# Kernel optimization log

Hardware: AMD Instinct MI355X
Metric: run time of the kernel (lower is better)

Reference implementation:

```python
import jax, jax.numpy as jnp
import numpy as np
import math

B, S, E, H = 2, 4096, 1024, 1024

def setup_inputs() -> dict:
    key = jax.random.key(0)
    ks = jax.random.split(key, 7)
    X = jax.random.normal(ks[0], (B, S, E), dtype=jnp.float32)
    attention_mask = jnp.ones((B, S, S), dtype=jnp.int32)
    sc = 1.0 / math.sqrt(E)
    Wq = jax.random.normal(ks[1], (H, E), dtype=jnp.float32) * sc
    Wk = jax.random.normal(ks[2], (H, E), dtype=jnp.float32) * sc
    Wv = jax.random.normal(ks[3], (H, E), dtype=jnp.float32) * sc
    bq = jnp.zeros((H,), dtype=jnp.float32)
    bk = jnp.zeros((H,), dtype=jnp.float32)
    bv = jnp.zeros((H,), dtype=jnp.float32)
    return {"X": X, "attention_mask": attention_mask,
            "Wq": Wq, "bq": bq, "Wk": Wk, "bk": bk, "Wv": Wv, "bv": bv}

def reference(X, attention_mask, Wq, bq, Wk, bk, Wv, bv):
    # Linear layers: y = x @ W^T + b (torch convention W is [out, in])
    Q = jnp.einsum('bse,he->bsh', X, Wq) + bq
    K = jnp.einsum('bse,he->bsh', X, Wk) + bk
    V = jnp.einsum('bse,he->bsh', X, Wv) + bv
    scale = 1.0 / math.sqrt(H)
    scores = jnp.einsum('bqh,bkh->bqk', Q, K) * scale  # [B,S,S]
    scores = jnp.where(attention_mask == 0, -jnp.inf, scores)
    # dropout (eval mode -> identity) would be applied here, BEFORE softmax
    weights = jax.nn.softmax(scores, axis=-1)
    out = jnp.einsum('bqk,bkh->bqh', weights, V)  # [B,S,H]
    return out
```

## Files before the change

kernel.cpp:

```cpp
#include <hip/hip_runtime.h>
#include <stdint.h>


typedef __bf16 bf16;
typedef __attribute__((ext_vector_type(4))) __bf16 bf16x4;
typedef __attribute__((ext_vector_type(8))) __bf16 bf16x8;
typedef __attribute__((ext_vector_type(4))) float f32x4;

__device__ __forceinline__ void g2l16(const void* g, void* l) {
  __builtin_amdgcn_global_load_lds(
      (const __attribute__((address_space(1))) uint32_t*)g,
      (__attribute__((address_space(3))) uint32_t*)l, 16, 0, 0);
}

__global__ __launch_bounds__(256) void cvt_f32_bf16(
    const float* __restrict__ src, bf16* __restrict__ dst, int n) {
  const int i = (blockIdx.x * 256 + threadIdx.x) * 8;
  if (i >= n) return;
  f32x4 a = *(const f32x4*)(src + i);
  f32x4 b = *(const f32x4*)(src + i + 4);
  bf16x8 o;
#pragma unroll
  for (int e = 0; e < 4; ++e) { o[e] = (bf16)a[e]; o[4 + e] = (bf16)b[e]; }
  *(bf16x8*)(dst + i) = o;
}

__global__ __launch_bounds__(256) void cvt_w3(
    const float* __restrict__ Wq, const float* __restrict__ Wk,
    const float* __restrict__ Wv, bf16* __restrict__ dst) {
  const int i = (blockIdx.x * 256 + threadIdx.x) * 8;
  const int seg = i >> 20;
  const int off = i & 1048575;
  const float* src = (seg == 0) ? Wq : (seg == 1) ? Wk : Wv;
  f32x4 a = *(const f32x4*)(src + off);
  f32x4 b = *(const f32x4*)(src + off + 4);
  bf16x8 o;
#pragma unroll
  for (int e = 0; e < 4; ++e) { o[e] = (bf16)a[e]; o[4 + e] = (bf16)b[e]; }
  *(bf16x8*)(dst + i) = o;
}


__global__ __launch_bounds__(256, 2) void gemm_qkv(
    const bf16* __restrict__ Xb, const bf16* __restrict__ Wb3,
    const float* __restrict__ bq, const float* __restrict__ bk,
    const float* __restrict__ bv, bf16* __restrict__ QK,
    bf16* __restrict__ Vt)
{
  constexpr int K = 1024, N = 1024;
  __shared__ __align__(16) bf16 ldsA[128 * 64];
  __shared__ __align__(16) bf16 ldsB[128 * 64];

  const int tid  = threadIdx.x;
  const int lane = tid & 63;
  const int wave = tid >> 6;
  const int which = blockIdx.y >> 3;
  const int n0 = (blockIdx.y & 7) * 128;
  const int m0 = blockIdx.x * 128;
  const bf16* Bt = Wb3 + (size_t)which * 1048576;
  const float* bias = (which == 0) ? bq : ((which == 1) ? bk : bv);

  const int l15  = lane & 15;
  const int quad = lane >> 4;
  const int wm = (wave >> 1) * 64;
  const int wn = (wave & 1) * 64;
  const int sw = l15 & 7;

  f32x4 acc[4][4];
#pragma unroll
  for (int i = 0; i < 4; ++i)
#pragma unroll
    for (int j = 0; j < 4; ++j) acc[i][j] = f32x4{0.f, 0.f, 0.f, 0.f};

  const int srow = tid >> 3;
  const int scol = ((tid & 7) ^ (srow & 7)) * 8;
  const size_t a_base = (size_t)(m0 + srow) * K + scol;
  const size_t b_base = (size_t)(n0 + srow) * K + scol;
  const int lds_off = tid * 8;

  for (int kt = 0; kt < K; kt += 64) {
    const bf16* ga = Xb + a_base + kt;
    const bf16* gb = Bt + b_base + kt;
#pragma unroll
    for (int it = 0; it < 4; ++it) {
      g2l16(ga + (size_t)(it * 32) * K, &ldsA[lds_off + it * 2048]);
      g2l16(gb + (size_t)(it * 32) * K, &ldsB[lds_off + it * 2048]);
    }
    __syncthreads();
#pragma unroll
    for (int ks = 0; ks < 2; ++ks) {
      const int ch = ks * 4 + quad;
      bf16x8 af[4], bfg[4];
#pragma unroll
      for (int i = 0; i < 4; ++i)
        af[i] = *(const bf16x8*)&ldsA[(wm + i * 16 + l15) * 64 + (ch ^ sw) * 8];
#pragma unroll
      for (int j = 0; j < 4; ++j)
        bfg[j] = *(const bf16x8*)&ldsB[(wn + j * 16 + l15) * 64 + (ch ^ sw) * 8];
#pragma unroll
      for (int i = 0; i < 4; ++i)
#pragma unroll
        for (int j = 0; j < 4; ++j)
          acc[i][j] = __builtin_amdgcn_mfma_f32_16x16x32_bf16(
              af[i], bfg[j], acc[i][j], 0, 0, 0);
    }
    __syncthreads();
  }

  if (which < 2) {
    bf16* C = QK + (size_t)which * (size_t)(8192 * 1024);
#pragma unroll
    for (int i = 0; i < 4; ++i) {
#pragma unroll
      for (int j = 0; j < 4; ++j) {
        const int r = m0 + wm + i * 16 + quad * 4;
        const int c = n0 + wn + j * 16 + l15;
        const float bvv = bias[c];
        f32x4 v = acc[i][j];
#pragma unroll
        for (int reg = 0; reg < 4; ++reg)
          C[(size_t)(r + reg) * N + c] = (bf16)(v[reg] + bvv);
      }
    }
  } else {
#pragma unroll
    for (int i = 0; i < 4; ++i) {
#pragma unroll
      for (int j = 0; j < 4; ++j) {
        const int r = m0 + wm + i * 16 + quad * 4;
        const int c = n0 + wn + j * 16 + l15;
        const int b = r >> 12, s = r & 4095;
        const float bvv = bias[c];
        f32x4 v = acc[i][j];
        bf16x4 o;
#pragma unroll
        for (int reg = 0; reg < 4; ++reg) o[reg] = (bf16)(v[reg] + bvv);
        *(bf16x4*)&Vt[((size_t)(b * 1024 + c)) * 4096 + s] = o;
      }
    }
  }
}

__global__ __launch_bounds__(256, 2) void gemm_scores(
    const bf16* __restrict__ A, const bf16* __restrict__ Bt,
    const int* __restrict__ mask, bf16* __restrict__ P,
    float* __restrict__ row_sum)
{
  constexpr int N = 4096, K = 1024;
  __shared__ __align__(16) bf16 ldsA[128 * 64];
  __shared__ __align__(16) bf16 ldsB[128 * 64];

  const int tid  = threadIdx.x;
  const int lane = tid & 63;
  const int wave = tid >> 6;
  const int m0 = blockIdx.x * 128;
  const int n0 = blockIdx.y * 128;
  const int batch = m0 >> 12;
  const bf16* Btb = Bt + (size_t)batch * (size_t)(4096 * 1024);

  const int l15  = lane & 15;
  const int quad = lane >> 4;
  const int wm = (wave >> 1) * 64;
  const int wn = (wave & 1) * 64;
  const int sw = l15 & 7;

  f32x4 acc[4][4];
#pragma unroll
  for (int i = 0; i < 4; ++i)
#pragma unroll
    for (int j = 0; j < 4; ++j) acc[i][j] = f32x4{0.f, 0.f, 0.f, 0.f};

  const int srow = tid >> 3;
  const int scol = ((tid & 7) ^ (srow & 7)) * 8;
  const size_t a_base = (size_t)(m0 + srow) * K + scol;
  const size_t b_base = (size_t)(n0 + srow) * K + scol;
  const int lds_off = tid * 8;

  for (int kt = 0; kt < K; kt += 64) {
    const bf16* ga = A + a_base + kt;
    const bf16* gb = Btb + b_base + kt;
#pragma unroll
    for (int it = 0; it < 4; ++it) {
      g2l16(ga + (size_t)(it * 32) * K, &ldsA[lds_off + it * 2048]);
      g2l16(gb + (size_t)(it * 32) * K, &ldsB[lds_off + it * 2048]);
    }
    __syncthreads();
#pragma unroll
    for (int ks = 0; ks < 2; ++ks) {
      const int ch = ks * 4 + quad;
      bf16x8 af[4], bfg[4];
#pragma unroll
      for (int i = 0; i < 4; ++i)
        af[i] = *(const bf16x8*)&ldsA[(wm + i * 16 + l15) * 64 + (ch ^ sw) * 8];
#pragma unroll
      for (int j = 0; j < 4; ++j)
        bfg[j] = *(const bf16x8*)&ldsB[(wn + j * 16 + l15) * 64 + (ch ^ sw) * 8];
#pragma unroll
      for (int i = 0; i < 4; ++i)
#pragma unroll
        for (int j = 0; j < 4; ++j)
          acc[i][j] = __builtin_amdgcn_mfma_f32_16x16x32_bf16(
              af[i], bfg[j], acc[i][j], 0, 0, 0);
    }
    __syncthreads();
  }

#pragma unroll
  for (int i = 0; i < 4; ++i) {
    const int r = m0 + wm + i * 16 + quad * 4;
    f32x4 rsum = f32x4{0.f, 0.f, 0.f, 0.f};
#pragma unroll
    for (int j = 0; j < 4; ++j) {
      const int c = n0 + wn + j * 16 + l15;
      f32x4 v = acc[i][j];
#pragma unroll
      for (int reg = 0; reg < 4; ++reg) {
        float e = __expf(v[reg] * 0.03125f);
        if (mask[(size_t)(r + reg) * N + c] == 0) e = 0.f;
        P[(size_t)(r + reg) * N + c] = (bf16)e;
        rsum[reg] += e;
      }
    }
#pragma unroll
    for (int off = 1; off < 16; off <<= 1) {
#pragma unroll
      for (int reg = 0; reg < 4; ++reg)
        rsum[reg] += __shfl_xor(rsum[reg], off);
    }
    if (l15 == 0) {
#pragma unroll
      for (int reg = 0; reg < 4; ++reg)
        atomicAdd(&row_sum[r + reg], rsum[reg]);
    }
  }
}

__global__ __launch_bounds__(256, 2) void gemm_pv(
    const bf16* __restrict__ A, const bf16* __restrict__ Bt,
    const float* __restrict__ row_sum, float* __restrict__ C)
{
  constexpr int N = 1024, K = 4096;
  __shared__ __align__(16) bf16 ldsA[128 * 64];
  __shared__ __align__(16) bf16 ldsB[128 * 64];

  const int tid  = threadIdx.x;
  const int lane = tid & 63;
  const int wave = tid >> 6;
  const int m0 = blockIdx.x * 128;
  const int n0 = blockIdx.y * 128;
  const int batch = m0 >> 12;
  const bf16* Btb = Bt + (size_t)batch * (size_t)(1024 * 4096);

  const int l15  = lane & 15;
  const int quad = lane >> 4;
  const int wm = (wave >> 1) * 64;
  const int wn = (wave & 1) * 64;
  const int sw = l15 & 7;

  f32x4 acc[4][4];
#pragma unroll
  for (int i = 0; i < 4; ++i)
#pragma unroll
    for (int j = 0; j < 4; ++j) acc[i][j] = f32x4{0.f, 0.f, 0.f, 0.f};

  const int srow = tid >> 3;
  const int scol = ((tid & 7) ^ (srow & 7)) * 8;
  const size_t a_base = (size_t)(m0 + srow) * K + scol;
  const size_t b_base = (size_t)(n0 + srow) * K + scol;
  const int lds_off = tid * 8;

  for (int kt = 0; kt < K; kt += 64) {
    const bf16* ga = A + a_base + kt;
    const bf16* gb = Btb + b_base + kt;
#pragma unroll
    for (int it = 0; it < 4; ++it) {
      g2l16(ga + (size_t)(it * 32) * K, &ldsA[lds_off + it * 2048]);
      g2l16(gb + (size_t)(it * 32) * K, &ldsB[lds_off + it * 2048]);
    }
    __syncthreads();
#pragma unroll
    for (int ks = 0; ks < 2; ++ks) {
      const int ch = ks * 4 + quad;
      bf16x8 af[4], bfg[4];
#pragma unroll
      for (int i = 0; i < 4; ++i)
        af[i] = *(const bf16x8*)&ldsA[(wm + i * 16 + l15) * 64 + (ch ^ sw) * 8];
#pragma unroll
      for (int j = 0; j < 4; ++j)
        bfg[j] = *(const bf16x8*)&ldsB[(wn + j * 16 + l15) * 64 + (ch ^ sw) * 8];
#pragma unroll
      for (int i = 0; i < 4; ++i)
#pragma unroll
        for (int j = 0; j < 4; ++j)
          acc[i][j] = __builtin_amdgcn_mfma_f32_16x16x32_bf16(
              af[i], bfg[j], acc[i][j], 0, 0, 0);
    }
    __syncthreads();
  }

#pragma unroll
  for (int i = 0; i < 4; ++i) {
    const int r = m0 + wm + i * 16 + quad * 4;
    f32x4 inv;
#pragma unroll
    for (int reg = 0; reg < 4; ++reg) inv[reg] = 1.0f / row_sum[r + reg];
#pragma unroll
    for (int j = 0; j < 4; ++j) {
      const int c = n0 + wn + j * 16 + l15;
      f32x4 v = acc[i][j];
#pragma unroll
      for (int reg = 0; reg < 4; ++reg)
        C[(size_t)(r + reg) * N + c] = v[reg] * inv[reg];
    }
  }
}

extern "C" void kernel_launch(void* const* d_in, const int* in_sizes, int n_in,
                              void* d_out, int out_size, void* d_ws,
                              size_t ws_size, hipStream_t stream) {
  const float* X   = (const float*)d_in[0];
  const int* mask  = (const int*)d_in[1];
  const float* Wq  = (const float*)d_in[2];
  const float* bq  = (const float*)d_in[3];
  const float* Wk  = (const float*)d_in[4];
  const float* bk  = (const float*)d_in[5];
  const float* Wv  = (const float*)d_in[6];
  const float* bv  = (const float*)d_in[7];
  float* out = (float*)d_out;

  const size_t QKV_ELEMS = (size_t)8192 * 1024;
  bf16* Q    = (bf16*)d_ws;
  bf16* Kb   = Q + QKV_ELEMS;
  bf16* X_bf = Kb + QKV_ELEMS;
  bf16* Vt   = X_bf + QKV_ELEMS;
  bf16* Sc   = Vt + QKV_ELEMS;
  bf16* W_bf = Sc;
  float* row_sum = (float*)X_bf;

  const dim3 blk(256);
  cvt_f32_bf16<<<dim3(4096), blk, 0, stream>>>(X, X_bf, 8388608);
  cvt_w3<<<dim3(1536), blk, 0, stream>>>(Wq, Wk, Wv, W_bf);
  gemm_qkv<<<dim3(64, 24), blk, 0, stream>>>(X_bf, W_bf, bq, bk, bv, Q, Vt);
  hipMemsetAsync(row_sum, 0, 8192 * sizeof(float), stream);
  gemm_scores<<<dim3(64, 32), blk, 0, stream>>>(Q, Kb, mask, Sc, row_sum);
  gemm_pv<<<dim3(64, 8), blk, 0, stream>>>(Sc, Vt, row_sum, out);
}
```

Measured before the change: 437.6 us.

## Unify GEMMs into a multi-stage pipelined k-loop with larger tiles and 8 waves

Replaces the three hand-written single-buffered GEMM loops with a shared templated k-loop. The new loop uses a 4-slot LDS ring with 3 stages in flight, explicit vmcnt waits, one barrier per 32-wide k step, and s_setprio around the MFMA block. Tiles grow to 256x128 or 256x256 with 512-thread blocks, which raises operand reuse and hides global-load latency behind compute. In exchange the kernels use more LDS and registers, which may cut occupancy, and the LDS XOR swizzle is dropped, so bank conflicts may return.

```diff
diff --git a/kernel.cpp b/kernel.cpp
--- a/kernel.cpp
+++ b/kernel.cpp
@@ -12,6 +12,16 @@
       (const __attribute__((address_space(1))) uint32_t*)g,
       (__attribute__((address_space(3))) uint32_t*)l, 16, 0, 0);
 }
+
+template <int N> __device__ __forceinline__ void waitvm() {
+  static_assert(N == 0 || N == 3 || N == 4 || N == 6 || N == 8, "vmcnt");
+  if constexpr (N == 0) asm volatile("s_waitcnt vmcnt(0)" ::: "memory");
+  else if constexpr (N == 3) asm volatile("s_waitcnt vmcnt(3)" ::: "memory");
+  else if constexpr (N == 4) asm volatile("s_waitcnt vmcnt(4)" ::: "memory");
+  else if constexpr (N == 6) asm volatile("s_waitcnt vmcnt(6)" ::: "memory");
+  else asm volatile("s_waitcnt vmcnt(8)" ::: "memory");
+}
+template <int V> struct IC { static constexpr int value = V; };
 
 __global__ __launch_bounds__(256) void cvt_f32_bf16(
     const float* __restrict__ src, bf16* __restrict__ dst, int n) {
@@ -40,96 +50,114 @@
   *(bf16x8*)(dst + i) = o;
 }
 
-
-__global__ __launch_bounds__(256, 2) void gemm_qkv(
+template <int BM, int BN, int WM, int WN, int NT>
+__device__ __forceinline__ void kloop(
+    const bf16* __restrict__ Ag, const bf16* __restrict__ Bg, const int K,
+    bf16* lds, f32x4 (&acc)[BM / WM / 16][BN / WN / 16]) {
+  constexpr int L = (BM + BN) / 128;
+  constexpr int MR = BM / WM / 16, NR = BN / WN / 16;
+  const int tid = threadIdx.x;
+  const int lane = tid & 63, wave = tid >> 6;
+  const int l15 = lane & 15, quad = lane >> 4;
+  const int wrow = (wave / WN) * (BM / WM);
+  const int wcol = (wave % WN) * (BN / WN);
+  const int srow = tid >> 2;
+  const int scol = (tid & 3) * 8;
+
+  auto stage = [&](int t) {
+    bf16* la = lds + (t & 3) * ((BM + BN) * 32);
+    bf16* lb = la + BM * 32;
+    const bf16* ga = Ag + (size_t)srow * K + t * 32 + scol;
+    const bf16* gb = Bg + (size_t)srow * K + t * 32 + scol;
+#pragma unroll
+    for (int r = 0; r < BM / 128; ++r)
+      g2l16(ga + (size_t)(r * 128) * K, la + (srow + r * 128) * 32 + scol);
+#pragma unroll
+    for (int r = 0; r < BN / 128; ++r)
+      g2l16(gb + (size_t)(r * 128) * K, lb + (srow + r * 128) * 32 + scol);
+  };
+
+  stage(0);
+  stage(1);
+  stage(2);
+
+  auto body = [&](int t, auto vm, bool do_stage) {
+    waitvm<decltype(vm)::value>();
+    __builtin_amdgcn_s_barrier();
+    if (do_stage) stage(t + 3);
+    const bf16* la = lds + (t & 3) * ((BM + BN) * 32);
+    const bf16* lb = la + BM * 32;
+    bf16x8 af[MR], bq[NR];
+#pragma unroll
+    for (int i = 0; i < MR; ++i)
+      af[i] = *(const bf16x8*)&la[(wrow + i * 16 + l15) * 32 + quad * 8];
+#pragma unroll
+    for (int j = 0; j < NR; ++j)
+      bq[j] = *(const bf16x8*)&lb[(wcol + j * 16 + l15) * 32 + quad * 8];
+    asm volatile("s_waitcnt lgkmcnt(0)" ::: "memory");
+    __builtin_amdgcn_s_setprio(1);
+#pragma unroll
+    for (int i = 0; i < MR; ++i)
+#pragma unroll
+      for (int j = 0; j < NR; ++j)
+        acc[i][j] = __builtin_amdgcn_mfma_f32_16x16x32_bf16(
+            af[i], bq[j], acc[i][j], 0, 0, 0);
+    __builtin_amdgcn_s_setprio(0);
+  };
+
+  for (int t = 0; t < NT - 2; ++t) body(t, IC<2 * L>{}, t + 3 < NT);
+  body(NT - 2, IC<L>{}, false);
+  body(NT - 1, IC<0>{}, false);
+}
+
+__global__ __launch_bounds__(512, 2) void gemm_qkv(
     const bf16* __restrict__ Xb, const bf16* __restrict__ Wb3,
     const float* __restrict__ bq, const float* __restrict__ bk,
     const float* __restrict__ bv, bf16* __restrict__ QK,
-    bf16* __restrict__ Vt)
-{
-  constexpr int K = 1024, N = 1024;
-  __shared__ __align__(16) bf16 ldsA[128 * 64];
-  __shared__ __align__(16) bf16 ldsB[128 * 64];
-
-  const int tid  = threadIdx.x;
-  const int lane = tid & 63;
-  const int wave = tid >> 6;
+    bf16* __restrict__ Vt) {
+  __shared__ __align__(16) bf16 lds[4 * 384 * 32];
   const int which = blockIdx.y >> 3;
   const int n0 = (blockIdx.y & 7) * 128;
-  const int m0 = blockIdx.x * 128;
-  const bf16* Bt = Wb3 + (size_t)which * 1048576;
+  const int m0 = blockIdx.x * 256;
+  const bf16* Ag = Xb + (size_t)m0 * 1024;
+  const bf16* Bg = Wb3 + (size_t)which * 1048576 + (size_t)n0 * 1024;
   const float* bias = (which == 0) ? bq : ((which == 1) ? bk : bv);
 
-  const int l15  = lane & 15;
-  const int quad = lane >> 4;
-  const int wm = (wave >> 1) * 64;
-  const int wn = (wave & 1) * 64;
-  const int sw = l15 & 7;
-
   f32x4 acc[4][4];
 #pragma unroll
   for (int i = 0; i < 4; ++i)
 #pragma unroll
     for (int j = 0; j < 4; ++j) acc[i][j] = f32x4{0.f, 0.f, 0.f, 0.f};
 
-  const int srow = tid >> 3;
-  const int scol = ((tid & 7) ^ (srow & 7)) * 8;
-  const size_t a_base = (size_t)(m0 + srow) * K + scol;
-  const size_t b_base = (size_t)(n0 + srow) * K + scol;
-  const int lds_off = tid * 8;
-
-  for (int kt = 0; kt < K; kt += 64) {
-    const bf16* ga = Xb + a_base + kt;
-    const bf16* gb = Bt + b_base + kt;
-#pragma unroll
-    for (int it = 0; it < 4; ++it) {
-      g2l16(ga + (size_t)(it * 32) * K, &ldsA[lds_off + it * 2048]);
-      g2l16(gb + (size_t)(it * 32) * K, &ldsB[lds_off + it * 2048]);
-    }
-    __syncthreads();
-#pragma unroll
-    for (int ks = 0; ks < 2; ++ks) {
-      const int ch = ks * 4 + quad;
-      bf16x8 af[4], bfg[4];
-#pragma unroll
-      for (int i = 0; i < 4; ++i)
-        af[i] = *(const bf16x8*)&ldsA[(wm + i * 16 + l15) * 64 + (ch ^ sw) * 8];
-#pragma unroll
-      for (int j = 0; j < 4; ++j)
-        bfg[j] = *(const bf16x8*)&ldsB[(wn + j * 16 + l15) * 64 + (ch ^ sw) * 8];
-#pragma unroll
-      for (int i = 0; i < 4; ++i)
-#pragma unroll
-        for (int j = 0; j < 4; ++j)
-          acc[i][j] = __builtin_amdgcn_mfma_f32_16x16x32_bf16(
-              af[i], bfg[j], acc[i][j], 0, 0, 0);
-    }
-    __syncthreads();
-  }
+  kloop<256, 128, 4, 2, 32>(Ag, Bg, 1024, lds, acc);
+
+  const int lane = threadIdx.x & 63, wave = threadIdx.x >> 6;
+  const int l15 = lane & 15, quad = lane >> 4;
+  const int wrow = (wave >> 1) * 64, wcol = (wave & 1) * 64;
 
   if (which < 2) {
     bf16* C = QK + (size_t)which * (size_t)(8192 * 1024);
 #pragma unroll
     for (int i = 0; i < 4; ++i) {
+      const int r = m0 + wrow + i * 16 + quad * 4;
 #pragma unroll
       for (int j = 0; j < 4; ++j) {
-        const int r = m0 + wm + i * 16 + quad * 4;
-        const int c = n0 + wn + j * 16 + l15;
+        const int c = n0 + wcol + j * 16 + l15;
         const float bvv = bias[c];
         f32x4 v = acc[i][j];
 #pragma unroll
         for (int reg = 0; reg < 4; ++reg)
-          C[(size_t)(r + reg) * N + c] = (bf16)(v[reg] + bvv);
+          C[(size_t)(r + reg) * 1024 + c] = (bf16)(v[reg] + bvv);
       }
     }
   } else {
 #pragma unroll
     for (int i = 0; i < 4; ++i) {
+      const int r = m0 + wrow + i * 16 + quad * 4;
+      const int b = r >> 12, s = r & 4095;
 #pragma unroll
       for (int j = 0; j < 4; ++j) {
-        const int r = m0 + wm + i * 16 + quad * 4;
-        const int c = n0 + wn + j * 16 + l15;
-        const int b = r >> 12, s = r & 4095;
+        const int c = n0 + wcol + j * 16 + l15;
         const float bvv = bias[c];
         f32x4 v = acc[i][j];
         bf16x4 o;
@@ -141,28 +169,69 @@
   }
 }
 
-__global__ __launch_bounds__(256, 2) void gemm_scores(
-    const bf16* __restrict__ A, const bf16* __restrict__ Bt,
+__global__ __launch_bounds__(512, 2) void gemm_scores(
+    const bf16* __restrict__ Q, const bf16* __restrict__ Kb,
     const int* __restrict__ mask, bf16* __restrict__ P,
-    float* __restrict__ row_sum)
-{
-  constexpr int N = 4096, K = 1024;
-  __shared__ __align__(16) bf16 ldsA[128 * 64];
-  __shared__ __align__(16) bf16 ldsB[128 * 64];
-
-  const int tid  = threadIdx.x;
-  const int lane = tid & 63;
-  const int wave = tid >> 6;
-  const int m0 = blockIdx.x * 128;
+    float* __restrict__ row_sum) {
+  __shared__ __align__(16) bf16 lds[4 * 512 * 32];
+  const int m0 = blockIdx.x * 256;
+  const int n0 = blockIdx.y * 256;
+  const int batch = m0 >> 12;
+  const bf16* Ag = Q + (size_t)m0 * 1024;
+  const bf16* Bg = Kb + (size_t)batch * (size_t)(4096 * 1024) +
+                   (size_t)n0 * 1024;
+
+  f32x4 acc[8][4];
+#pragma unroll
+  for (int i = 0; i < 8; ++i)
+#pragma unroll
+    for (int j = 0; j < 4; ++j) acc[i][j] = f32x4{0.f, 0.f, 0.f, 0.f};
+
+  kloop<256, 256, 2, 4, 32>(Ag, Bg, 1024, lds, acc);
+
+  const int lane = threadIdx.x & 63, wave = threadIdx.x >> 6;
+  const int l15 = lane & 15, quad = lane >> 4;
+  const int wrow = (wave >> 2) * 128, wcol = (wave & 3) * 64;
+
+#pragma unroll
+  for (int i = 0; i < 8; ++i) {
+    const int r = m0 + wrow + i * 16 + quad * 4;
+    f32x4 rsum = f32x4{0.f, 0.f, 0.f, 0.f};
+#pragma unroll
+    for (int j = 0; j < 4; ++j) {
+      const int c = n0 + wcol + j * 16 + l15;
+      f32x4 v = acc[i][j];
+#pragma unroll
+      for (int reg = 0; reg < 4; ++reg) {
+        float e = __expf(v[reg] * 0.03125f);
+        if (mask[(size_t)(r + reg) * 4096 + c] == 0) e = 0.f;
+        P[(size_t)(r + reg) * 4096 + c] = (bf16)e;
+        rsum[reg] += e;
+      }
+    }
+#pragma unroll
+    for (int off = 1; off < 16; off <<= 1) {
+#pragma unroll
+      for (int reg = 0; reg < 4; ++reg)
+        rsum[reg] += __shfl_xor(rsum[reg], off);
+    }
+    if (l15 == 0) {
+#pragma unroll
+      for (int reg = 0; reg < 4; ++reg)
+        atomicAdd(&row_sum[r + reg], rsum[reg]);
+    }
+  }
+}
+
+__global__ __launch_bounds__(512, 2) void gemm_pv(
+    const bf16* __restrict__ Pm, const bf16* __restrict__ Vt,
+    const float* __restrict__ row_sum, float* __restrict__ C) {
+  __shared__ __align__(16) bf16 lds[4 * 384 * 32];
+  const int m0 = blockIdx.x * 256;
   const int n0 = blockIdx.y * 128;
   const int batch = m0 >> 12;
-  const bf16* Btb = Bt + (size_t)batch * (size_t)(4096 * 1024);
-
-  const int l15  = lane & 15;
-  const int quad = lane >> 4;
-  const int wm = (wave >> 1) * 64;
-  const int wn = (wave & 1) * 64;
-  const int sw = l15 & 7;
+  const bf16* Ag = Pm + (size_t)m0 * 4096;
+  const bf16* Bg = Vt + ((size_t)batch * 1024 + n0) * 4096;
 
   f32x4 acc[4][4];
 #pragma unroll
@@ -170,147 +239,26 @@
 #pragma unroll
     for (int j = 0; j < 4; ++j) acc[i][j] = f32x4{0.f, 0.f, 0.f, 0.f};
 
-  const int srow = tid >> 3;
-  const int scol = ((tid & 7) ^ (srow & 7)) * 8;
-  const size_t a_base = (size_t)(m0 + srow) * K + scol;
-  const size_t b_base = (size_t)(n0 + srow) * K + scol;
-  const int lds_off = tid * 8;
-
-  for (int kt = 0; kt < K; kt += 64) {
-    const bf16* ga = A + a_base + kt;
-    const bf16* gb = Btb + b_base + kt;
-#pragma unroll
-    for (int it = 0; it < 4; ++it) {
-      g2l16(ga + (size_t)(it * 32) * K, &ldsA[lds_off + it * 2048]);
-      g2l16(gb + (size_t)(it * 32) * K, &ldsB[lds_off + it * 2048]);
-    }
-    __syncthreads();
-#pragma unroll
-    for (int ks = 0; ks < 2; ++ks) {
-      const int ch = ks * 4 + quad;
-      bf16x8 af[4], bfg[4];
-#pragma unroll
-      for (int i = 0; i < 4; ++i)
-        af[i] = *(const bf16x8*)&ldsA[(wm + i * 16 + l15) * 64 + (ch ^ sw) * 8];
-#pragma unroll
-      for (int j = 0; j < 4; ++j)
-        bfg[j] = *(const bf16x8*)&ldsB[(wn + j * 16 + l15) * 64 + (ch ^ sw) * 8];
-#pragma unroll
-      for (int i = 0; i < 4; ++i)
-#pragma unroll
-        for (int j = 0; j < 4; ++j)
-          acc[i][j] = __builtin_amdgcn_mfma_f32_16x16x32_bf16(
-              af[i], bfg[j], acc[i][j], 0, 0, 0);
-    }
-    __syncthreads();
-  }
+  kloop<256, 128, 4, 2, 128>(Ag, Bg, 4096, lds, acc);
+
+  const int lane = threadIdx.x & 63, wave = threadIdx.x >> 6;
+  const int l15 = lane & 15, quad = lane >> 4;
+  const int wrow = (wave >> 1) * 64, wcol = (wave & 1) * 64;
 
 #pragma unroll
   for (int i = 0; i < 4; ++i) {
-    const int r = m0 + wm + i * 16 + quad * 4;
-    f32x4 rsum = f32x4{0.f, 0.f, 0.f, 0.f};
+    const int r = m0 + wrow + i * 16 + quad * 4;
+    const f32x4 rs = *(const f32x4*)&row_sum[r];
+    f32x4 inv;
+#pragma unroll
+    for (int reg = 0; reg < 4; ++reg) inv[reg] = 1.0f / rs[reg];
 #pragma unroll
     for (int j = 0; j < 4; ++j) {
-      const int c = n0 + wn + j * 16 + l15;
+      const int c = n0 + wcol + j * 16 + l15;
       f32x4 v = acc[i][j];
 #pragma unroll
-      for (int reg = 0; reg < 4; ++reg) {
-        float e = __expf(v[reg] * 0.03125f);
-        if (mask[(size_t)(r + reg) * N + c] == 0) e = 0.f;
-        P[(size_t)(r + reg) * N + c] = (bf16)e;
-        rsum[reg] += e;
-      }
-    }
-#pragma unroll
-    for (int off = 1; off < 16; off <<= 1) {
-#pragma unroll
       for (int reg = 0; reg < 4; ++reg)
-        rsum[reg] += __shfl_xor(rsum[reg], off);
-    }
-    if (l15 == 0) {
-#pragma unroll
-      for (int reg = 0; reg < 4; ++reg)
-        atomicAdd(&row_sum[r + reg], rsum[reg]);
-    }
-  }
-}
-
-__global__ __launch_bounds__(256, 2) void gemm_pv(
-    const bf16* __restrict__ A, const bf16* __restrict__ Bt,
-    const float* __restrict__ row_sum, float* __restrict__ C)
-{
-  constexpr int N = 1024, K = 4096;
-  __shared__ __align__(16) bf16 ldsA[128 * 64];
-  __shared__ __align__(16) bf16 ldsB[128 * 64];
-
-  const int tid  = threadIdx.x;
-  const int lane = tid & 63;
-  const int wave = tid >> 6;
-  const int m0 = blockIdx.x * 128;
-  const int n0 = blockIdx.y * 128;
-  const int batch = m0 >> 12;
-  const bf16* Btb = Bt + (size_t)batch * (size_t)(1024 * 4096);
-
-  const int l15  = lane & 15;
-  const int quad = lane >> 4;
-  const int wm = (wave >> 1) * 64;
-  const int wn = (wave & 1) * 64;
-  const int sw = l15 & 7;
-
-  f32x4 acc[4][4];
-#pragma unroll
-  for (int i = 0; i < 4; ++i)
-#pragma unroll
-    for (int j = 0; j < 4; ++j) acc[i][j] = f32x4{0.f, 0.f, 0.f, 0.f};
-
-  const int srow = tid >> 3;
-  const int scol = ((tid & 7) ^ (srow & 7)) * 8;
-  const size_t a_base = (size_t)(m0 + srow) * K + scol;
-  const size_t b_base = (size_t)(n0 + srow) * K + scol;
-  const int lds_off = tid * 8;
-
-  for (int kt = 0; kt < K; kt += 64) {
-    const bf16* ga = A + a_base + kt;
-    const bf16* gb = Btb + b_base + kt;
-#pragma unroll
-    for (int it = 0; it < 4; ++it) {
-      g2l16(ga + (size_t)(it * 32) * K, &ldsA[lds_off + it * 2048]);
-      g2l16(gb + (size_t)(it * 32) * K, &ldsB[lds_off + it * 2048]);
-    }
-    __syncthreads();
-#pragma unroll
-    for (int ks = 0; ks < 2; ++ks) {
-      const int ch = ks * 4 + quad;
-      bf16x8 af[4], bfg[4];
-#pragma unroll
-      for (int i = 0; i < 4; ++i)
-        af[i] = *(const bf16x8*)&ldsA[(wm + i * 16 + l15) * 64 + (ch ^ sw) * 8];
-#pragma unroll
-      for (int j = 0; j < 4; ++j)
-        bfg[j] = *(const bf16x8*)&ldsB[(wn + j * 16 + l15) * 64 + (ch ^ sw) * 8];
-#pragma unroll
-      for (int i = 0; i < 4; ++i)
-#pragma unroll
-        for (int j = 0; j < 4; ++j)
-          acc[i][j] = __builtin_amdgcn_mfma_f32_16x16x32_bf16(
-              af[i], bfg[j], acc[i][j], 0, 0, 0);
-    }
-    __syncthreads();
-  }
-
-#pragma unroll
-  for (int i = 0; i < 4; ++i) {
-    const int r = m0 + wm + i * 16 + quad * 4;
-    f32x4 inv;
-#pragma unroll
-    for (int reg = 0; reg < 4; ++reg) inv[reg] = 1.0f / row_sum[r + reg];
-#pragma unroll
-    for (int j = 0; j < 4; ++j) {
-      const int c = n0 + wn + j * 16 + l15;
-      f32x4 v = acc[i][j];
-#pragma unroll
-      for (int reg = 0; reg < 4; ++reg)
-        C[(size_t)(r + reg) * N + c] = v[reg] * inv[reg];
+        C[(size_t)(r + reg) * 1024 + c] = v[reg] * inv[reg];
     }
   }
 }
@@ -337,11 +285,12 @@
   bf16* W_bf = Sc;
   float* row_sum = (float*)X_bf;
 
-  const dim3 blk(256);
-  cvt_f32_bf16<<<dim3(4096), blk, 0, stream>>>(X, X_bf, 8388608);
-  cvt_w3<<<dim3(1536), blk, 0, stream>>>(Wq, Wk, Wv, W_bf);
-  gemm_qkv<<<dim3(64, 24), blk, 0, stream>>>(X_bf, W_bf, bq, bk, bv, Q, Vt);
+  cvt_f32_bf16<<<dim3(4096), dim3(256), 0, stream>>>(X, X_bf, 8388608);
+  cvt_w3<<<dim3(1536), dim3(256), 0, stream>>>(Wq, Wk, Wv, W_bf);
+  gemm_qkv<<<dim3(32, 24), dim3(512), 0, stream>>>(X_bf, W_bf, bq, bk, bv, Q,
+                                                   Vt);
   hipMemsetAsync(row_sum, 0, 8192 * sizeof(float), stream);
-  gemm_scores<<<dim3(64, 32), blk, 0, stream>>>(Q, Kb, mask, Sc, row_sum);
-  gemm_pv<<<dim3(64, 8), blk, 0, stream>>>(Sc, Vt, row_sum, out);
-}
+  gemm_scores<<<dim3(32, 16), dim3(512), 0, stream>>>(Q, Kb, mask, Sc,
+                                                      row_sum);
+  gemm_pv<<<dim3(32, 8), dim3(512), 0, stream>>>(Sc, Vt, row_sum, out);
+}
```

After: 442.2 us. No clear change (+1.0%).

## Rewrite scores GEMM as 256x256 double-buffered pipelined tile with block swizzling

Applied to the files above, without the earlier changes.

Replaces the scores GEMM with a 512-thread, 256x256-tile kernel. Its K loop double-buffers LDS, issues staggered global-to-LDS loads in phases alongside MFMA work, and uses explicit waitcnt, barrier and setprio control. This is meant to hide load latency and raise data reuse per tile. The QKV and PV GEMMs get a block-index remap for L2 locality and a larger launch_bounds occupancy hint. The hand-written waitcnt scheduling is fragile, and 128KB of LDS per block limits occupancy.

```diff
diff --git a/kernel.cpp b/kernel.cpp
--- a/kernel.cpp
+++ b/kernel.cpp
@@ -11,6 +11,21 @@
   __builtin_amdgcn_global_load_lds(
       (const __attribute__((address_space(1))) uint32_t*)g,
       (__attribute__((address_space(3))) uint32_t*)l, 16, 0, 0);
+}
+
+__device__ __forceinline__ f32x4 ds_read128(uint32_t addr) {
+  f32x4 d;
+  asm volatile("ds_read_b128 %0, %1" : "=v"(d) : "v"(addr));
+  return d;
+}
+
+template <int V> struct IC { static constexpr int value = V; };
+template <bool V> struct BC { static constexpr bool value = V; };
+
+template <int N> __device__ __forceinline__ void waitvm() {
+  if constexpr (N == 6) asm volatile("s_waitcnt vmcnt(6)" ::: "memory");
+  else if constexpr (N == 4) asm volatile("s_waitcnt vmcnt(4)" ::: "memory");
+  else if constexpr (N == 0) asm volatile("s_waitcnt vmcnt(0)" ::: "memory");
 }
 
 __global__ __launch_bounds__(256) void cvt_f32_bf16(
@@ -40,8 +55,118 @@
   *(bf16x8*)(dst + i) = o;
 }
 
-
-__global__ __launch_bounds__(256, 2) void gemm_qkv(
+template <int NT>
+__device__ __forceinline__ void kloop256(
+    const bf16* __restrict__ Ag, const bf16* __restrict__ Bg, const int KA,
+    const int KB, bf16* lds, f32x4 (&acc)[8][4]) {
+  const int tid = threadIdx.x;
+  const int lane = tid & 63;
+  const int wave = tid >> 6;
+  const int l15 = lane & 15, quad = lane >> 4;
+  const int wrow = (wave >> 2) * 128;
+  const int wcol = (wave & 3) * 64;
+  const int srow = tid >> 3;
+  const int scol = ((tid & 7) ^ (srow & 7)) * 8;
+  const int swz = l15 & 7;
+
+  const uint32_t lds_u = (uint32_t)(uintptr_t)lds;
+  const uint32_t a_l15 = lds_u + (uint32_t)((wrow + l15) * 128);
+  const uint32_t b_l15 = lds_u + 32768u + (uint32_t)((wcol + l15) * 128);
+  const uint32_t ck0 = (uint32_t)(((quad) ^ swz) * 16);
+  const uint32_t ck1 = (uint32_t)(((4 + quad) ^ swz) * 16);
+
+  auto stg = [&](int t, int h) {
+    bf16* base = lds + (t & 1) * 32768;
+    if (h == 0) {
+      const bf16* g = Bg + (size_t)srow * KB + t * 64 + scol;
+      g2l16(g, base + 16384 + tid * 8);
+      g2l16(g + (size_t)64 * KB, base + 16384 + tid * 8 + 4096);
+    } else if (h == 1) {
+      const bf16* g = Bg + (size_t)(128 + srow) * KB + t * 64 + scol;
+      g2l16(g, base + 24576 + tid * 8);
+      g2l16(g + (size_t)64 * KB, base + 24576 + tid * 8 + 4096);
+    } else if (h == 2) {
+      const bf16* g = Ag + (size_t)srow * KA + t * 64 + scol;
+      g2l16(g, base + tid * 8);
+      g2l16(g + (size_t)128 * KA, base + tid * 8 + 8192);
+    } else {
+      const bf16* g = Ag + (size_t)(64 + srow) * KA + t * 64 + scol;
+      g2l16(g, base + 4096 + tid * 8);
+      g2l16(g + (size_t)128 * KA, base + 4096 + tid * 8 + 8192);
+    }
+  };
+
+  f32x4 brf[2][4];
+  auto phase = [&](int t, auto qc, int st, int sh, auto dsc, auto vmc) {
+    constexpr int q = decltype(qc)::value;
+    constexpr bool ds = decltype(dsc)::value;
+    constexpr int vm = decltype(vmc)::value;
+    const uint32_t bb = (t & 1) ? 65536u : 0u;
+    f32x4 ar[2][2];
+#pragma unroll
+    for (int i = 0; i < 2; ++i) {
+      ar[i][0] = ds_read128(a_l15 + bb + (uint32_t)((2 * q + i) * 2048) + ck0);
+      ar[i][1] = ds_read128(a_l15 + bb + (uint32_t)((2 * q + i) * 2048) + ck1);
+    }
+    if constexpr (q == 0) {
+#pragma unroll
+      for (int j = 0; j < 4; ++j) {
+        brf[0][j] = ds_read128(b_l15 + bb + (uint32_t)(j * 2048) + ck0);
+        brf[1][j] = ds_read128(b_l15 + bb + (uint32_t)(j * 2048) + ck1);
+      }
+    }
+    if constexpr (ds) stg(st, sh);
+    __builtin_amdgcn_s_barrier();
+    asm volatile("s_waitcnt lgkmcnt(0)" ::: "memory");
+    __builtin_amdgcn_sched_barrier(0);
+    __builtin_amdgcn_s_setprio(1);
+#pragma unroll
+    for (int ks = 0; ks < 2; ++ks)
+#pragma unroll
+      for (int i = 0; i < 2; ++i)
+#pragma unroll
+        for (int j = 0; j < 4; ++j)
+          acc[2 * q + i][j] = __builtin_amdgcn_mfma_f32_16x16x32_bf16(
+              __builtin_bit_cast(bf16x8, ar[i][ks]),
+              __builtin_bit_cast(bf16x8, brf[ks][j]),
+              acc[2 * q + i][j], 0, 0, 0);
+    __builtin_amdgcn_s_setprio(0);
+    waitvm<vm>();
+    __builtin_amdgcn_s_barrier();
+  };
+
+  stg(0, 0); stg(0, 1); stg(0, 2); stg(0, 3);
+  stg(1, 0); stg(1, 1); stg(1, 2);
+  asm volatile("s_waitcnt vmcnt(6)" ::: "memory");
+  __builtin_amdgcn_s_barrier();
+
+  constexpr int NI = NT / 2;
+#pragma unroll 1
+  for (int u = 0; u < NI - 1; ++u) {
+    const int t0 = 2 * u, t1 = t0 + 1;
+    phase(t0, IC<0>{}, t1, 3, BC<true>{}, IC<-1>{});
+    phase(t0, IC<1>{}, t0 + 2, 0, BC<true>{}, IC<-1>{});
+    phase(t0, IC<2>{}, t0 + 2, 1, BC<true>{}, IC<-1>{});
+    phase(t0, IC<3>{}, t0 + 2, 2, BC<true>{}, IC<6>{});
+    phase(t1, IC<0>{}, t0 + 2, 3, BC<true>{}, IC<-1>{});
+    phase(t1, IC<1>{}, t0 + 3, 0, BC<true>{}, IC<-1>{});
+    phase(t1, IC<2>{}, t0 + 3, 1, BC<true>{}, IC<-1>{});
+    phase(t1, IC<3>{}, t0 + 3, 2, BC<true>{}, IC<6>{});
+  }
+  {
+    const int t0 = NT - 2, t1 = NT - 1;
+    phase(t0, IC<0>{}, t1, 3, BC<true>{}, IC<-1>{});
+    phase(t0, IC<1>{}, 0, 0, BC<false>{}, IC<-1>{});
+    phase(t0, IC<2>{}, 0, 0, BC<false>{}, IC<-1>{});
+    phase(t0, IC<3>{}, 0, 0, BC<false>{}, IC<0>{});
+    phase(t1, IC<0>{}, 0, 0, BC<false>{}, IC<-1>{});
+    phase(t1, IC<1>{}, 0, 0, BC<false>{}, IC<-1>{});
+    phase(t1, IC<2>{}, 0, 0, BC<false>{}, IC<-1>{});
+    phase(t1, IC<3>{}, 0, 0, BC<false>{}, IC<-1>{});
+  }
+}
+
+__global__ __launch_bounds__(256, 4) void gemm_qkv(
     const bf16* __restrict__ Xb, const bf16* __restrict__ Wb3,
     const float* __restrict__ bq, const float* __restrict__ bk,
     const float* __restrict__ bv, bf16* __restrict__ QK,
@@ -54,9 +179,12 @@
   const int tid  = threadIdx.x;
   const int lane = tid & 63;
   const int wave = tid >> 6;
-  const int which = blockIdx.y >> 3;
-  const int n0 = (blockIdx.y & 7) * 128;
-  const int m0 = blockIdx.x * 128;
+  const int bid = blockIdx.y * 64 + blockIdx.x;
+  const int sb = (bid & 7) * 192 + (bid >> 3);
+  const int bx = sb & 63, by = sb >> 6;
+  const int which = by >> 3;
+  const int n0 = (by & 7) * 128;
+  const int m0 = bx * 128;
   const bf16* Bt = Wb3 + (size_t)which * 1048576;
   const float* bias = (which == 0) ? bq : ((which == 1) ? bk : bv);
 
@@ -141,83 +269,46 @@
   }
 }
 
-__global__ __launch_bounds__(256, 2) void gemm_scores(
-    const bf16* __restrict__ A, const bf16* __restrict__ Bt,
+__global__ __launch_bounds__(512, 2) void gemm_scores(
+    const bf16* __restrict__ Q, const bf16* __restrict__ Kb,
     const int* __restrict__ mask, bf16* __restrict__ P,
-    float* __restrict__ row_sum)
-{
-  constexpr int N = 4096, K = 1024;
-  __shared__ __align__(16) bf16 ldsA[128 * 64];
-  __shared__ __align__(16) bf16 ldsB[128 * 64];
-
-  const int tid  = threadIdx.x;
-  const int lane = tid & 63;
-  const int wave = tid >> 6;
-  const int m0 = blockIdx.x * 128;
-  const int n0 = blockIdx.y * 128;
+    float* __restrict__ row_sum) {
+  __shared__ __align__(16) bf16 lds[2 * 32768];
+  const int bid = blockIdx.y * 32 + blockIdx.x;
+  const int sb = (bid & 7) * 64 + (bid >> 3);
+  const int bx = sb & 31, by = sb >> 5;
+  const int m0 = bx * 256;
+  const int n0 = by * 256;
   const int batch = m0 >> 12;
-  const bf16* Btb = Bt + (size_t)batch * (size_t)(4096 * 1024);
-
-  const int l15  = lane & 15;
-  const int quad = lane >> 4;
-  const int wm = (wave >> 1) * 64;
-  const int wn = (wave & 1) * 64;
-  const int sw = l15 & 7;
-
-  f32x4 acc[4][4];
-#pragma unroll
-  for (int i = 0; i < 4; ++i)
+  const bf16* Ag = Q + (size_t)m0 * 1024;
+  const bf16* Bg = Kb + (size_t)batch * (size_t)(4096 * 1024) +
+                   (size_t)n0 * 1024;
+
+  f32x4 acc[8][4];
+#pragma unroll
+  for (int i = 0; i < 8; ++i)
 #pragma unroll
     for (int j = 0; j < 4; ++j) acc[i][j] = f32x4{0.f, 0.f, 0.f, 0.f};
 
-  const int srow = tid >> 3;
-  const int scol = ((tid & 7) ^ (srow & 7)) * 8;
-  const size_t a_base = (size_t)(m0 + srow) * K + scol;
-  const size_t b_base = (size_t)(n0 + srow) * K + scol;
-  const int lds_off = tid * 8;
-
-  for (int kt = 0; kt < K; kt += 64) {
-    const bf16* ga = A + a_base + kt;
-    const bf16* gb = Btb + b_base + kt;
-#pragma unroll
-    for (int it = 0; it < 4; ++it) {
-      g2l16(ga + (size_t)(it * 32) * K, &ldsA[lds_off + it * 2048]);
-      g2l16(gb + (size_t)(it * 32) * K, &ldsB[lds_off + it * 2048]);
-    }
-    __syncthreads();
-#pragma unroll
-    for (int ks = 0; ks < 2; ++ks) {
-      const int ch = ks * 4 + quad;
-      bf16x8 af[4], bfg[4];
-#pragma unroll
-      for (int i = 0; i < 4; ++i)
-        af[i] = *(const bf16x8*)&ldsA[(wm + i * 16 + l15) * 64 + (ch ^ sw) * 8];
-#pragma unroll
-      for (int j = 0; j < 4; ++j)
-        bfg[j] = *(const bf16x8*)&ldsB[(wn + j * 16 + l15) * 64 + (ch ^ sw) * 8];
-#pragma unroll
-      for (int i = 0; i < 4; ++i)
-#pragma unroll
-        for (int j = 0; j < 4; ++j)
-          acc[i][j] = __builtin_amdgcn_mfma_f32_16x16x32_bf16(
-              af[i], bfg[j], acc[i][j], 0, 0, 0);
-    }
-    __syncthreads();
-  }
-
-#pragma unroll
-  for (int i = 0; i < 4; ++i) {
-    const int r = m0 + wm + i * 16 + quad * 4;
+  kloop256<16>(Ag, Bg, 1024, 1024, lds, acc);
+
+  const int lane = threadIdx.x & 63, wave = threadIdx.x >> 6;
+  const int l15 = lane & 15, quad = lane >> 4;
+  const int wrow = (wave >> 2) * 128, wcol = (wave & 3) * 64;
+
+#pragma unroll
+  for (int i = 0; i < 8; ++i) {
+    const int r = m0 + wrow + i * 16 + quad * 4;
     f32x4 rsum = f32x4{0.f, 0.f, 0.f, 0.f};
 #pragma unroll
     for (int j = 0; j < 4; ++j) {
-      const int c = n0 + wn + j * 16 + l15;
+      const int c = n0 + wcol + j * 16 + l15;
       f32x4 v = acc[i][j];
 #pragma unroll
       for (int reg = 0; reg < 4; ++reg) {
         float e = __expf(v[reg] * 0.03125f);
-        if (mask[(size_t)(r + reg) * N + c] == 0) e = 0.f;
-        P[(size_t)(r + reg) * N + c] = (bf16)e;
+        if (mask[(size_t)(r + reg) * 4096 + c] == 0) e = 0.f;
+        P[(size_t)(r + reg) * 4096 + c] = (bf16)e;
         rsum[reg] += e;
       }
     }
@@ -235,7 +326,7 @@
   }
 }
 
-__global__ __launch_bounds__(256, 2) void gemm_pv(
+__global__ __launch_bounds__(256, 4) void gemm_pv(
     const bf16* __restrict__ A, const bf16* __restrict__ Bt,
     const float* __restrict__ row_sum, float* __restrict__ C)
 {
@@ -246,8 +337,11 @@
   const int tid  = threadIdx.x;
   const int lane = tid & 63;
   const int wave = tid >> 6;
-  const int m0 = blockIdx.x * 128;
-  const int n0 = blockIdx.y * 128;
+  const int bid = blockIdx.y * 64 + blockIdx.x;
+  const int sb = (bid & 7) * 64 + (bid >> 3);
+  const int bx = sb & 63, by = sb >> 6;
+  const int m0 = bx * 128;
+  const int n0 = by * 128;
   const int batch = m0 >> 12;
   const bf16* Btb = Bt + (size_t)batch * (size_t)(1024 * 4096);
 
@@ -337,11 +431,12 @@
   bf16* W_bf = Sc;
   float* row_sum = (float*)X_bf;
 
-  const dim3 blk(256);
-  cvt_f32_bf16<<<dim3(4096), blk, 0, stream>>>(X, X_bf, 8388608);
-  cvt_w3<<<dim3(1536), blk, 0, stream>>>(Wq, Wk, Wv, W_bf);
-  gemm_qkv<<<dim3(64, 24), blk, 0, stream>>>(X_bf, W_bf, bq, bk, bv, Q, Vt);
+  cvt_f32_bf16<<<dim3(4096), dim3(256), 0, stream>>>(X, X_bf, 8388608);
+  cvt_w3<<<dim3(1536), dim3(256), 0, stream>>>(Wq, Wk, Wv, W_bf);
+  gemm_qkv<<<dim3(64, 24), dim3(256), 0, stream>>>(X_bf, W_bf, bq, bk, bv, Q,
+                                                   Vt);
   hipMemsetAsync(row_sum, 0, 8192 * sizeof(float), stream);
-  gemm_scores<<<dim3(64, 32), blk, 0, stream>>>(Q, Kb, mask, Sc, row_sum);
-  gemm_pv<<<dim3(64, 8), blk, 0, stream>>>(Sc, Vt, row_sum, out);
-}
+  gemm_scores<<<dim3(32, 16), dim3(512), 0, stream>>>(Q, Kb, mask, Sc,
+                                                      row_sum);
+  gemm_pv<<<dim3(64, 8), dim3(256), 0, stream>>>(Sc, Vt, row_sum, out);
+}
```

Result: slower. 517.7 us (+18.3%).
